# Kernel optimization log

Measured on AMD Instinct MI355X. Metric: run time of the kernel, lower is better.

## Reference

```python
import jax, jax.numpy as jnp
import numpy as np

EPS = 1e-05  # norm_epsilon

def setup_inputs() -> dict:
    key = jax.random.key(0)
    ks = jax.random.split(key, 6)
    B, T, D, E, N, C = 16, 512, 256, 16, 8192, 1
    xs = jax.random.normal(ks[0], (B, T, D), jnp.float32)
    pad_mask = jnp.ones((B, T), dtype=bool)
    masked_masks = jax.random.randint(ks[1], (B, T), 0, 2) > 0
    ln_gamma = jnp.ones((D,), jnp.float32)
    ln_beta = jnp.zeros((D,), jnp.float32)
    # xavier_normal init for the (frozen) random projection
    projection = jax.random.normal(ks[2], (D, E), jnp.float32) * (2.0 / (D + E)) ** 0.5
    embeddings = jax.random.normal(ks[3], (C, E, N), jnp.float32)
    top_n_out = jax.random.normal(ks[4], (C, D, N), jnp.float32) * 0.02
    mask_emb = jax.random.normal(ks[5], (D,), jnp.float32) * 0.1
    return {"xs": xs, "pad_mask": pad_mask, "masked_masks": masked_masks,
            "ln_gamma": ln_gamma, "ln_beta": ln_beta, "projection": projection,
            "embeddings": embeddings, "top_n_out": top_n_out, "mask_emb": mask_emb}

def reference(xs, pad_mask, masked_masks, ln_gamma, ln_beta, projection, embeddings, top_n_out, mask_emb):
    B, T, D = xs.shape
    C = embeddings.shape[0]
    # ---- target path: layer norm -> random projection -> nearest codebook idx ----
    mu = jnp.mean(xs, -1, keepdims=True)
    var = jnp.mean((xs - mu) ** 2, -1, keepdims=True)
    h = (xs - mu) / jnp.sqrt(var + EPS) * ln_gamma + ln_beta
    proj = jnp.einsum('btd,de->bte', h, projection).reshape(B * T, -1)  # [BT,E]
    # pairwise squared distances: [C, BT, N]
    dist = (jnp.sum(proj ** 2, axis=1)[None, :, None]
            + jnp.sum(embeddings ** 2, axis=1)[:, None, :]
            - 2.0 * jnp.einsum('te,cen->ctn', proj, embeddings))
    target = jnp.argmin(dist, axis=-1).T.reshape(B, T, C)  # [B,T,C] int
    # ---- masked input -> encoder (identity stand-in) -> per-codebook logits ----
    masked_xs = jnp.where(masked_masks[..., None], mask_emb, xs)
    logits = jnp.einsum('btd,cdn->btcn', masked_xs, top_n_out)  # [B,T,C,N]
    logp = jax.nn.log_softmax(logits, axis=-1)
    ce = -jnp.take_along_axis(logp, target[..., None], axis=-1)[..., 0]  # [B,T,C]
    m = (pad_mask & masked_masks).astype(logits.dtype)  # [B,T]
    loss = jnp.sum(ce * m[..., None]) / (jnp.sum(m) * C)
    return loss
```

## Files before the change

kernel.cpp:

```cpp
#include <hip/hip_runtime.h>
#include <hip/hip_bf16.h>
#include <math.h>

#define BT   8192
#define DD   256
#define EE   16
#define NN   8192

typedef __attribute__((ext_vector_type(8))) short short8;
typedef __attribute__((ext_vector_type(4))) float f32x4;

__device__ __forceinline__ unsigned short f2bf(float x) {
  union { float f; unsigned int u; } c; c.f = x;
  unsigned int r = (c.u + 0x7FFFu + ((c.u >> 16) & 1u)) >> 16;
  return (unsigned short)r;
}
__device__ __forceinline__ unsigned int ordf(float d) {
  union { float f; unsigned int u; } c; c.f = d;
  return ((int)c.u < 0) ? ~c.u : (c.u | 0x80000000u);
}
__device__ __forceinline__ unsigned long long shflxor64(unsigned long long v, int m) {
  unsigned int lo = (unsigned int)v, hi = (unsigned int)(v >> 32);
  lo = __shfl_xor((int)lo, m);
  hi = __shfl_xor((int)hi, m);
  return ((unsigned long long)hi << 32) | lo;
}
__device__ __forceinline__ void gload_lds16(const void* g, void* l) {
  __builtin_amdgcn_global_load_lds((const __attribute__((address_space(1))) void*)g,
                                   (__attribute__((address_space(3))) void*)l, 16, 0, 0);
}

#define XT_LD 65
__global__ __launch_bounds__(256) void k_pre(const float* __restrict__ xs,
                                             const int* __restrict__ mm,
                                             const float* __restrict__ memb,
                                             const float* __restrict__ gamma,
                                             const float* __restrict__ beta,
                                             const float* __restrict__ P,
                                             const float* __restrict__ W,
                                             const float* __restrict__ emb,
                                             unsigned short* __restrict__ xmb,
                                             unsigned short* __restrict__ projb,
                                             unsigned short* __restrict__ Wt,
                                             unsigned short* __restrict__ embT,
                                             float* __restrict__ sqe,
                                             unsigned long long* __restrict__ keys,
                                             float* __restrict__ sumexp) {
  __shared__ __align__(16) float xt[32 * XT_LD * 4];
  __shared__ float stats[32][2];
  int bid = blockIdx.x;
  int tid = threadIdx.x;

  if (bid < 512) {
    int n0 = (bid & 127) * 64;
    int d0 = (bid >> 7) * 64;
    #pragma unroll
    for (int pass = 0; pass < 16; pass++) {
      int idx = pass * 256 + tid;
      int dd = idx >> 6, ln = idx & 63;
      xt[ln * 65 + dd] = W[(size_t)(d0 + dd) * NN + n0 + ln];
    }
    __syncthreads();
    #pragma unroll
    for (int pass = 0; pass < 2; pass++) {
      int g = pass * 256 + tid;
      int row = g >> 3, c8 = g & 7;
      short8 v;
      #pragma unroll
      for (int i = 0; i < 8; i++) v[i] = (short)f2bf(xt[row * 65 + c8 * 8 + i]);
      *(short8*)(Wt + (size_t)(n0 + row) * DD + d0 + c8 * 8) = v;
    }
    return;
  }
  if (bid < 544) {
    int n = (bid - 512) * 256 + tid;
    float e[EE];
    float sq = 0.f;
    #pragma unroll
    for (int k = 0; k < EE; k++) { e[k] = emb[k * NN + n]; sq += e[k] * e[k]; }
    short8 lo, hi;
    #pragma unroll
    for (int k = 0; k < 8; k++) { lo[k] = (short)f2bf(e[k]); hi[k] = (short)f2bf(e[k + 8]); }
    *(short8*)(embT + (size_t)n * EE)     = lo;
    *(short8*)(embT + (size_t)n * EE + 8) = hi;
    sqe[n] = sq;
    keys[n] = ~0ULL;
    return;
  }
  int pb = bid - 544;
  int t0 = pb * 32;
  int w = tid >> 6;
  int col4 = tid & 63;
  float4 mb4 = ((const float4*)memb)[col4];

  #pragma unroll
  for (int j = 0; j < 8; j++) {
    int k = tid + j * 256;
    int row = w + j * 4;
    float4 xv = ((const float4*)xs)[(size_t)pb * 2048 + k];
    int m = mm[t0 + row];
    float4 v = m ? mb4 : xv;
    ushort2 o01 = { f2bf(v.x), f2bf(v.y) };
    ushort2 o23 = { f2bf(v.z), f2bf(v.w) };
    ((ushort2*)(xmb + (size_t)(t0 + row) * DD + col4 * 4))[0] = o01;
    ((ushort2*)(xmb + (size_t)(t0 + row) * DD + col4 * 4))[1] = o23;
    *(float4*)&xt[(row * XT_LD + col4) * 4] = xv;
  }
  __syncthreads();
  {
    int t = tid >> 3, g = tid & 7;
    float s = 0.f, s2 = 0.f;
    #pragma unroll
    for (int i = 0; i < 8; i++) {
      float4 v = *(const float4*)&xt[(t * XT_LD + g * 8 + i) * 4];
      s  += v.x + v.y + v.z + v.w;
      s2 += v.x * v.x + v.y * v.y + v.z * v.z + v.w * v.w;
    }
    #pragma unroll
    for (int m = 1; m <= 4; m <<= 1) { s += __shfl_xor(s, m); s2 += __shfl_xor(s2, m); }
    if (g == 0) {
      float mu = s * (1.0f / DD);
      float var = s2 * (1.0f / DD) - mu * mu;
      stats[t][0] = mu;
      stats[t][1] = rsqrtf(var + 1e-5f);
    }
  }
  if (tid < 32) sumexp[t0 + tid] = 0.f;
  __syncthreads();
  {
    int t = tid >> 3, e0 = (tid & 7) * 2;
    float mu = stats[t][0], rstd = stats[t][1];
    float a0 = 0.f, a1 = 0.f;
    for (int d = 0; d < DD; d += 4) {
      float4 xv = *(const float4*)&xt[(t * XT_LD + (d >> 2)) * 4];
      float xd[4] = { xv.x, xv.y, xv.z, xv.w };
      #pragma unroll
      for (int dd = 0; dd < 4; dd++) {
        float h = (xd[dd] - mu) * rstd * gamma[d + dd] + beta[d + dd];
        a0 += h * P[(d + dd) * EE + e0];
        a1 += h * P[(d + dd) * EE + e0 + 1];
      }
    }
    ushort2 o = { f2bf(a0), f2bf(a1) };
    *(ushort2*)(projb + (size_t)(t0 + t) * EE + e0) = o;
  }
}

#define NS4 8
#define ASEG (NN / NS4)
__global__ __launch_bounds__(256) void k_argmin(const unsigned short* __restrict__ projb,
                                                const unsigned short* __restrict__ embT,
                                                const float* __restrict__ sqe,
                                                unsigned long long* __restrict__ keys) {
  int tid = threadIdx.x;
  int w = tid >> 6, lane = tid & 63;
  int q = lane >> 4, c = lane & 15;
  int tw = blockIdx.x * 64 + w * 16;
  int nseg = blockIdx.y * ASEG;

  short8 a = {0, 0, 0, 0, 0, 0, 0, 0};
  if (q < 2) a = *(const short8*)(projb + (size_t)(tw + c) * EE + q * 8);

  unsigned long long bk[4];
  #pragma unroll
  for (int r = 0; r < 4; r++) bk[r] = ~0ULL;

  #pragma unroll 2
  for (int it = 0; it < ASEG / 16; it++) {
    int n = nseg + it * 16 + c;
    short8 b = {0, 0, 0, 0, 0, 0, 0, 0};
    if (q < 2) b = *(const short8*)(embT + (size_t)n * EE + q * 8);
    float sq = sqe[n];
    f32x4 acc = (f32x4){0.f, 0.f, 0.f, 0.f};
    acc = __builtin_amdgcn_mfma_f32_16x16x32_bf16(a, b, acc, 0, 0, 0);
    #pragma unroll
    for (int r = 0; r < 4; r++) {
      float dist = sq - 2.f * acc[r];
      unsigned long long key = ((unsigned long long)ordf(dist) << 32) | (unsigned int)n;
      bk[r] = key < bk[r] ? key : bk[r];
    }
  }
  #pragma unroll
  for (int r = 0; r < 4; r++) {
    #pragma unroll
    for (int m = 1; m <= 8; m <<= 1) {
      unsigned long long o = shflxor64(bk[r], m);
      bk[r] = o < bk[r] ? o : bk[r];
    }
  }
  if (c == 0) {
    #pragma unroll
    for (int r = 0; r < 4; r++)
      atomicMin(&keys[tw + q * 4 + r], bk[r]);
  }
}

__global__ __launch_bounds__(256, 4) void k_ce5(const unsigned short* __restrict__ xmb,
                                                const unsigned short* __restrict__ Wt,
                                                const unsigned long long* __restrict__ keys,
                                                float* __restrict__ sumexp,
                                                float* __restrict__ ltar) {
  __shared__ __align__(16) unsigned short ldsA[2][128 * 32];
  __shared__ __align__(16) unsigned short ldsB[2][128 * 32];
  int tid = threadIdx.x;
  int lane = tid & 63;
  int w = tid >> 6;
  int q = lane >> 4, c = lane & 15;
  int wm = w >> 1, wn = w & 1;
  int t0 = blockIdx.x * 128;
  int n0 = blockIdx.y * 128;
  int sw = q ^ ((c >> 1) & 3);

  f32x4 acc[4][4];
  #pragma unroll
  for (int mi = 0; mi < 4; mi++)
    #pragma unroll
    for (int ni = 0; ni < 4; ni++) acc[mi][ni] = (f32x4){0.f, 0.f, 0.f, 0.f};

  #define STAGE(buf, itv) do {                                                  \
    int kk_ = (itv) * 32;                                                       \
    _Pragma("unroll")                                                           \
    for (int j = 0; j < 2; j++) {                                               \
      int g = j * 256 + tid;                                                    \
      int row = g >> 2;                                                         \
      int qg = (g & 3) ^ ((g >> 3) & 3);                                        \
      gload_lds16(xmb + (size_t)(t0 + row) * DD + kk_ + qg * 8,                 \
                  ldsA[buf] + g * 8);                                           \
      gload_lds16(Wt + (size_t)(n0 + row) * DD + kk_ + qg * 8,                  \
                  ldsB[buf] + g * 8);                                           \
    }                                                                           \
  } while (0)

  STAGE(0, 0);
  __syncthreads();

  #pragma unroll
  for (int it = 0; it < 8; it++) {
    int cur = it & 1;
    if (it < 7) STAGE(cur ^ 1, it + 1);

    short8 a[4], b[4];
    #pragma unroll
    for (int mi = 0; mi < 4; mi++)
      a[mi] = *(const short8*)(ldsA[cur] + (wm * 64 + mi * 16 + c) * 32 + sw * 8);
    #pragma unroll
    for (int ni = 0; ni < 4; ni++)
      b[ni] = *(const short8*)(ldsB[cur] + (wn * 64 + ni * 16 + c) * 32 + sw * 8);
    #pragma unroll
    for (int mi = 0; mi < 4; mi++)
      #pragma unroll
      for (int ni = 0; ni < 4; ni++)
        acc[mi][ni] = __builtin_amdgcn_mfma_f32_16x16x32_bf16(a[mi], b[ni], acc[mi][ni], 0, 0, 0);

    if (it < 7) __syncthreads();
  }
  #undef STAGE

  #pragma unroll
  for (int mi = 0; mi < 4; mi++) {
    int rowb = t0 + wm * 64 + mi * 16 + q * 4;
    int tg[4];
    float rs[4];
    #pragma unroll
    for (int r = 0; r < 4; r++) {
      tg[r] = (int)(unsigned int)(keys[rowb + r] & 0xFFFFFFFFULL);
      rs[r] = 0.f;
    }
    #pragma unroll
    for (int ni = 0; ni < 4; ni++) {
      int col = n0 + wn * 64 + ni * 16 + c;
      #pragma unroll
      for (int r = 0; r < 4; r++) {
        float v = acc[mi][ni][r];
        if (col == tg[r])
          ltar[rowb + r] = v;
        rs[r] += __expf(v);
      }
    }
    #pragma unroll
    for (int r = 0; r < 4; r++) {
      float s = rs[r];
      s += __shfl_xor(s, 1);
      s += __shfl_xor(s, 2);
      s += __shfl_xor(s, 4);
      s += __shfl_xor(s, 8);
      if (c == 0)
        atomicAdd(&sumexp[rowb + r], s);
    }
  }
}

__global__ __launch_bounds__(1024) void k_final(const float* __restrict__ sumexp,
                                                const float* __restrict__ ltar,
                                                const int* __restrict__ padm,
                                                const int* __restrict__ mm,
                                                float* __restrict__ out) {
  int tid = threadIdx.x;
  float sum = 0.f, cnt = 0.f;
  for (int t = tid; t < BT; t += 1024) {
    float ce = __logf(sumexp[t]) - ltar[t];
    if (padm[t] && mm[t]) { sum += ce; cnt += 1.f; }
  }
  #pragma unroll
  for (int off = 32; off; off >>= 1) { sum += __shfl_down(sum, off); cnt += __shfl_down(cnt, off); }
  __shared__ float rs[16], rc[16];
  int wid = tid >> 6, lane = tid & 63;
  if (lane == 0) { rs[wid] = sum; rc[wid] = cnt; }
  __syncthreads();
  if (tid == 0) {
    float S = 0.f, Cn = 0.f;
    for (int i = 0; i < 16; i++) { S += rs[i]; Cn += rc[i]; }
    out[0] = S / Cn;
  }
}

extern "C" void kernel_launch(void* const* d_in, const int* in_sizes, int n_in,
                              void* d_out, int out_size, void* d_ws, size_t ws_size,
                              hipStream_t stream) {
  const float* xs    = (const float*)d_in[0];
  const int*   padm  = (const int*)d_in[1];
  const int*   mm    = (const int*)d_in[2];
  const float* gamma = (const float*)d_in[3];
  const float* beta  = (const float*)d_in[4];
  const float* P     = (const float*)d_in[5];
  const float* emb   = (const float*)d_in[6];
  const float* W     = (const float*)d_in[7];
  const float* memb  = (const float*)d_in[8];
  float* out = (float*)d_out;

  char* ws = (char*)d_ws;
  size_t off = 0;
  unsigned short* xmb   = (unsigned short*)(ws + off); off += (size_t)BT * DD * 2;
  unsigned short* Wtb   = (unsigned short*)(ws + off); off += (size_t)NN * DD * 2;
  unsigned short* embT  = (unsigned short*)(ws + off); off += (size_t)NN * EE * 2;
  unsigned short* projb = (unsigned short*)(ws + off); off += (size_t)BT * EE * 2;
  float* sqe            = (float*)(ws + off);          off += (size_t)NN * 4;
  unsigned long long* keys = (unsigned long long*)(ws + off); off += (size_t)BT * 8;
  float* sumexp         = (float*)(ws + off);          off += (size_t)BT * 4;
  float* ltar           = (float*)(ws + off);          off += (size_t)BT * 4;

  k_pre   <<<800, 256, 0, stream>>>(xs, mm, memb, gamma, beta, P, W, emb,
                                    xmb, projb, Wtb, embT, sqe, keys, sumexp);
  k_argmin<<<dim3(BT / 64, NS4), 256, 0, stream>>>(projb, embT, sqe, keys);
  k_ce5   <<<dim3(64, 64), 256, 0, stream>>>(xmb, Wtb, keys, sumexp, ltar);
  k_final <<<1, 1024, 0, stream>>>(sumexp, ltar, padm, mm, out);
}
```

Measured before the change: 183.8 us.

## Triple-buffer CE GEMM LDS and enlarge tile to 256 rows with 512 threads

The cross-entropy GEMM kernel now uses 512 threads covering a 256x128 output tile, so each loaded Wt tile is reused across twice as many rows. LDS buffering goes from double to triple, with two stages prefetched ahead. Explicit vmcnt waits plus raw barriers replace __syncthreads so loads stay in flight across iterations. B fragments are loaded per column inside the MFMA loop to lower register pressure. The cost is more LDS per block (about 72 KB) and fewer blocks, which may lower occupancy, and the hand-coded vmcnt counts must match the number of issued loads.

```diff
diff --git a/kernel.cpp b/kernel.cpp
--- a/kernel.cpp
+++ b/kernel.cpp
@@ -195,19 +195,19 @@
   }
 }
 
-__global__ __launch_bounds__(256, 4) void k_ce5(const unsigned short* __restrict__ xmb,
+__global__ __launch_bounds__(512, 4) void k_ce5(const unsigned short* __restrict__ xmb,
                                                 const unsigned short* __restrict__ Wt,
                                                 const unsigned long long* __restrict__ keys,
                                                 float* __restrict__ sumexp,
                                                 float* __restrict__ ltar) {
-  __shared__ __align__(16) unsigned short ldsA[2][128 * 32];
-  __shared__ __align__(16) unsigned short ldsB[2][128 * 32];
+  __shared__ __align__(16) unsigned short ldsA[3][256 * 32];
+  __shared__ __align__(16) unsigned short ldsB[3][128 * 32];
   int tid = threadIdx.x;
   int lane = tid & 63;
   int w = tid >> 6;
   int q = lane >> 4, c = lane & 15;
   int wm = w >> 1, wn = w & 1;
-  int t0 = blockIdx.x * 128;
+  int t0 = blockIdx.x * 256;
   int n0 = blockIdx.y * 128;
   int sw = q ^ ((c >> 1) & 3);
 
@@ -221,38 +221,55 @@
     int kk_ = (itv) * 32;                                                       \
     _Pragma("unroll")                                                           \
     for (int j = 0; j < 2; j++) {                                               \
-      int g = j * 256 + tid;                                                    \
+      int g = j * 512 + tid;                                                    \
       int row = g >> 2;                                                         \
       int qg = (g & 3) ^ ((g >> 3) & 3);                                        \
       gload_lds16(xmb + (size_t)(t0 + row) * DD + kk_ + qg * 8,                 \
                   ldsA[buf] + g * 8);                                           \
+    }                                                                           \
+    {                                                                           \
+      int g = tid;                                                              \
+      int row = g >> 2;                                                         \
+      int qg = (g & 3) ^ ((g >> 3) & 3);                                        \
       gload_lds16(Wt + (size_t)(n0 + row) * DD + kk_ + qg * 8,                  \
                   ldsB[buf] + g * 8);                                           \
     }                                                                           \
   } while (0)
 
   STAGE(0, 0);
-  __syncthreads();
+  STAGE(1, 1);
+  asm volatile("s_waitcnt vmcnt(3)" ::: "memory");
+  __builtin_amdgcn_s_barrier();
 
   #pragma unroll
   for (int it = 0; it < 8; it++) {
-    int cur = it & 1;
-    if (it < 7) STAGE(cur ^ 1, it + 1);
-
-    short8 a[4], b[4];
+    const int cur = it % 3;
+    const int nxt = (it + 2) % 3;
+    if (it + 2 < 8) {
+      if (nxt == 0)      STAGE(0, it + 2);
+      else if (nxt == 1) STAGE(1, it + 2);
+      else               STAGE(2, it + 2);
+    }
+
+    short8 a[4];
     #pragma unroll
     for (int mi = 0; mi < 4; mi++)
       a[mi] = *(const short8*)(ldsA[cur] + (wm * 64 + mi * 16 + c) * 32 + sw * 8);
     #pragma unroll
-    for (int ni = 0; ni < 4; ni++)
-      b[ni] = *(const short8*)(ldsB[cur] + (wn * 64 + ni * 16 + c) * 32 + sw * 8);
-    #pragma unroll
-    for (int mi = 0; mi < 4; mi++)
+    for (int ni = 0; ni < 4; ni++) {
+      short8 b = *(const short8*)(ldsB[cur] + (wn * 64 + ni * 16 + c) * 32 + sw * 8);
       #pragma unroll
-      for (int ni = 0; ni < 4; ni++)
-        acc[mi][ni] = __builtin_amdgcn_mfma_f32_16x16x32_bf16(a[mi], b[ni], acc[mi][ni], 0, 0, 0);
-
-    if (it < 7) __syncthreads();
+      for (int mi = 0; mi < 4; mi++)
+        acc[mi][ni] = __builtin_amdgcn_mfma_f32_16x16x32_bf16(a[mi], b, acc[mi][ni], 0, 0, 0);
+    }
+
+    if (it < 6) {
+      asm volatile("s_waitcnt vmcnt(3)" ::: "memory");
+      __builtin_amdgcn_s_barrier();
+    } else if (it == 6) {
+      asm volatile("s_waitcnt vmcnt(0)" ::: "memory");
+      __builtin_amdgcn_s_barrier();
+    }
   }
   #undef STAGE
 
@@ -342,6 +359,6 @@
   k_pre   <<<800, 256, 0, stream>>>(xs, mm, memb, gamma, beta, P, W, emb,
                                     xmb, projb, Wtb, embT, sqe, keys, sumexp);
   k_argmin<<<dim3(BT / 64, NS4), 256, 0, stream>>>(projb, embT, sqe, keys);
-  k_ce5   <<<dim3(64, 64), 256, 0, stream>>>(xmb, Wtb, keys, sumexp, ltar);
+  k_ce5   <<<dim3(32, 64), 512, 0, stream>>>(xmb, Wtb, keys, sumexp, ltar);
   k_final <<<1, 1024, 0, stream>>>(sumexp, ltar, padm, mm, out);
 }
```

New measurement: 176.0 us. 1.04x faster.
